# Performance work log

Measured on AMD Instinct MI355X. Metric: run time of the kernel, lower is better.

## Reference

```python
import jax, jax.numpy as jnp
import numpy as np


def setup_inputs() -> dict:
    key = jax.random.key(0)
    B, F, D = 16384, 26, 32
    inputs = jax.random.normal(key, (B, F, D), dtype=jnp.float32)
    return {"inputs": inputs}


def reference(inputs) -> jnp.ndarray:
    # inputs: [B, F, D]. Output: [B, F*(F-1)/2, D] of pairwise elementwise products,
    # ordered as (i, j) with i < j, i outer loop, j inner loop (matches tf double loop).
    F = inputs.shape[1]
    i_idx, j_idx = np.triu_indices(F, k=1)  # row-major order == original loop order
    # Single fused gather-multiply over index pairs.
    return inputs[:, i_idx, :] * inputs[:, j_idx, :]
```

## Files before the change

kernel.cpp:

```cpp
#include <hip/hip_runtime.h>

#define NF 26
#define ND 32
#define NPAIR 325
#define ROW_F4 (NF * ND / 4)
#define OUT_F4 (NPAIR * ND / 4)

__global__ __launch_bounds__(256) void interaction_kernel(
    const float4* __restrict__ in, float4* __restrict__ out)
{
    __shared__ float4 s_row[ROW_F4];
    __shared__ short  s_ai[NPAIR];
    __shared__ short  s_bj[NPAIR];

    const int b   = blockIdx.x;
    const int tid = threadIdx.x;

    if (tid < ROW_F4) s_row[tid] = in[b * ROW_F4 + tid];

    for (int p = tid; p < NPAIR; p += 256) {
        int i = 0, s = 0;
        while (s + (NF - 1 - i) <= p) { s += NF - 1 - i; ++i; }
        int j = p - s + i + 1;
        s_ai[p] = (short)(i * (ND / 4));
        s_bj[p] = (short)(j * (ND / 4));
    }
    __syncthreads();

    const int base = b * OUT_F4;
    for (int q = tid; q < OUT_F4; q += 256) {
        const int p  = q >> 3;
        const int d4 = q & 7;
        const float4 a = s_row[s_ai[p] + d4];
        const float4 v = s_row[s_bj[p] + d4];
        float4 r;
        r.x = a.x * v.x;
        r.y = a.y * v.y;
        r.z = a.z * v.z;
        r.w = a.w * v.w;
        out[base + q] = r;
    }
}

extern "C" void kernel_launch(void* const* d_in, const int* in_sizes, int n_in,
                              void* d_out, int out_size, void* d_ws, size_t ws_size,
                              hipStream_t stream) {
    const float4* in  = (const float4*)d_in[0];
    float4*       out = (float4*)d_out;
    const int B = in_sizes[0] / (NF * ND);
    interaction_kernel<<<B, 256, 0, stream>>>(in, out);
}
```

Baseline: 147.6 us.

## Process four rows per block with constant pair table and nontemporal stores

Replaces the per-block runtime computation of pair indices with a compile-time table in constant memory, and keeps each thread's source offsets in registers. Each block now handles four batch rows, which amortizes the table lookup and block setup. Output writes use nontemporal stores to reduce cache pollution on the large streaming output. The launch assumes the batch is divisible by four and gives fewer blocks, which lowers parallelism.

```diff
diff --git a/kernel.cpp b/kernel.cpp
--- a/kernel.cpp
+++ b/kernel.cpp
@@ -5,48 +5,74 @@
 #define NPAIR 325
 #define ROW_F4 (NF * ND / 4)
 #define OUT_F4 (NPAIR * ND / 4)
+#define ROWS 4
+#define NTHREADS 256
+#define KFULL (OUT_F4 / NTHREADS)
+#define KTAIL (OUT_F4 % NTHREADS)
 
-__global__ __launch_bounds__(256) void interaction_kernel(
-    const float4* __restrict__ in, float4* __restrict__ out)
+typedef float f32x4 __attribute__((ext_vector_type(4)));
+
+struct PairTab { unsigned short v[NPAIR]; };
+constexpr PairTab make_tab() {
+    PairTab t{};
+    int n = 0;
+    for (int i = 0; i < NF; ++i)
+        for (int j = i + 1; j < NF; ++j)
+            t.v[n++] = (unsigned short)((i * (ND / 4)) | ((j * (ND / 4)) << 8));
+    return t;
+}
+__constant__ PairTab c_tab = make_tab();
+
+__global__ __launch_bounds__(NTHREADS) void interaction_kernel(
+    const f32x4* __restrict__ in, f32x4* __restrict__ out)
 {
-    __shared__ float4 s_row[ROW_F4];
-    __shared__ short  s_ai[NPAIR];
-    __shared__ short  s_bj[NPAIR];
+    __shared__ f32x4 s_row[ROWS * ROW_F4];
 
-    const int b   = blockIdx.x;
+    const int b0  = blockIdx.x * ROWS;
     const int tid = threadIdx.x;
 
-    if (tid < ROW_F4) s_row[tid] = in[b * ROW_F4 + tid];
+    const f32x4* src = in + (size_t)b0 * ROW_F4;
+    for (int t = tid; t < ROWS * ROW_F4; t += NTHREADS)
+        s_row[t] = src[t];
 
-    for (int p = tid; p < NPAIR; p += 256) {
-        int i = 0, s = 0;
-        while (s + (NF - 1 - i) <= p) { s += NF - 1 - i; ++i; }
-        int j = p - s + i + 1;
-        s_ai[p] = (short)(i * (ND / 4));
-        s_bj[p] = (short)(j * (ND / 4));
+    int aoff[KFULL + 1], boff[KFULL + 1];
+    #pragma unroll
+    for (int k = 0; k <= KFULL; ++k) {
+        const int q = (k < KFULL) ? (tid + k * NTHREADS)
+                                  : (KFULL * NTHREADS + (tid < KTAIL ? tid : 0));
+        const unsigned int t = c_tab.v[q >> 3];
+        const int d = q & 7;
+        aoff[k] = (int)(t & 0xffu) + d;
+        boff[k] = (int)(t >> 8) + d;
     }
+
     __syncthreads();
 
-    const int base = b * OUT_F4;
-    for (int q = tid; q < OUT_F4; q += 256) {
-        const int p  = q >> 3;
-        const int d4 = q & 7;
-        const float4 a = s_row[s_ai[p] + d4];
-        const float4 v = s_row[s_bj[p] + d4];
-        float4 r;
-        r.x = a.x * v.x;
-        r.y = a.y * v.y;
-        r.z = a.z * v.z;
-        r.w = a.w * v.w;
-        out[base + q] = r;
+    #pragma unroll 1
+    for (int r = 0; r < ROWS; ++r) {
+        const f32x4* __restrict__ row = s_row + r * ROW_F4;
+        f32x4* __restrict__ dst = out + (size_t)(b0 + r) * OUT_F4;
+        #pragma unroll
+        for (int k = 0; k < KFULL; ++k) {
+            const f32x4 a = row[aoff[k]];
+            const f32x4 v = row[boff[k]];
+            const f32x4 rr = a * v;
+            __builtin_nontemporal_store(rr, dst + tid + k * NTHREADS);
+        }
+        if (tid < KTAIL) {
+            const f32x4 a = row[aoff[KFULL]];
+            const f32x4 v = row[boff[KFULL]];
+            const f32x4 rr = a * v;
+            __builtin_nontemporal_store(rr, dst + KFULL * NTHREADS + tid);
+        }
     }
 }
 
 extern "C" void kernel_launch(void* const* d_in, const int* in_sizes, int n_in,
                               void* d_out, int out_size, void* d_ws, size_t ws_size,
                               hipStream_t stream) {
-    const float4* in  = (const float4*)d_in[0];
-    float4*       out = (float4*)d_out;
+    const f32x4* in  = (const f32x4*)d_in[0];
+    f32x4*       out = (f32x4*)d_out;
     const int B = in_sizes[0] / (NF * ND);
-    interaction_kernel<<<B, 256, 0, stream>>>(in, out);
+    interaction_kernel<<<B / ROWS, NTHREADS, 0, stream>>>(in, out);
 }
```

New measurement: 141.6 us. 4.1% less time.

## Compute pair products from registers per row with nontemporal stores

Applied to the files above, without the earlier changes.

Replaces the shared-memory staging and index tables with a per-thread register copy of one row's 26 float4 slices. The pair loop is fully unrolled so each thread writes its product directly. Output is written with nontemporal stores to avoid polluting caches, and each wave handles 8 rows. This removes the LDS traffic, the syncthreads and the index computation, at the cost of higher register use and a grid that assumes B is divisible by 32.

```diff
diff --git a/kernel.cpp b/kernel.cpp
--- a/kernel.cpp
+++ b/kernel.cpp
@@ -5,48 +5,46 @@
 #define NPAIR 325
 #define ROW_F4 (NF * ND / 4)
 #define OUT_F4 (NPAIR * ND / 4)
+#define ROWS_PER_WAVE 8
+#define NTHREADS 256
+#define ROWS_PER_BLOCK (ROWS_PER_WAVE * NTHREADS / 64)
 
-__global__ __launch_bounds__(256) void interaction_kernel(
-    const float4* __restrict__ in, float4* __restrict__ out)
+typedef float f32x4 __attribute__((ext_vector_type(4)));
+
+__global__ __launch_bounds__(NTHREADS) void interaction_kernel(
+    const f32x4* __restrict__ in, f32x4* __restrict__ out)
 {
-    __shared__ float4 s_row[ROW_F4];
-    __shared__ short  s_ai[NPAIR];
-    __shared__ short  s_bj[NPAIR];
+    const int tid  = threadIdx.x;
+    const int wave = tid >> 6;
+    const int lane = tid & 63;
+    const int r    = lane >> 3;
+    const int d4   = lane & 7;
 
-    const int b   = blockIdx.x;
-    const int tid = threadIdx.x;
+    const long row = (long)blockIdx.x * ROWS_PER_BLOCK + wave * ROWS_PER_WAVE + r;
 
-    if (tid < ROW_F4) s_row[tid] = in[b * ROW_F4 + tid];
+    const f32x4* __restrict__ src = in + row * ROW_F4 + d4;
+    f32x4 a[NF];
+    #pragma unroll
+    for (int f = 0; f < NF; ++f) a[f] = src[f * (ND / 4)];
 
-    for (int p = tid; p < NPAIR; p += 256) {
-        int i = 0, s = 0;
-        while (s + (NF - 1 - i) <= p) { s += NF - 1 - i; ++i; }
-        int j = p - s + i + 1;
-        s_ai[p] = (short)(i * (ND / 4));
-        s_bj[p] = (short)(j * (ND / 4));
-    }
-    __syncthreads();
-
-    const int base = b * OUT_F4;
-    for (int q = tid; q < OUT_F4; q += 256) {
-        const int p  = q >> 3;
-        const int d4 = q & 7;
-        const float4 a = s_row[s_ai[p] + d4];
-        const float4 v = s_row[s_bj[p] + d4];
-        float4 r;
-        r.x = a.x * v.x;
-        r.y = a.y * v.y;
-        r.z = a.z * v.z;
-        r.w = a.w * v.w;
-        out[base + q] = r;
+    f32x4* __restrict__ dst = out + row * OUT_F4 + d4;
+    int p = 0;
+    #pragma unroll
+    for (int i = 0; i < NF; ++i) {
+        #pragma unroll
+        for (int j = i + 1; j < NF; ++j) {
+            __builtin_nontemporal_store(a[i] * a[j], dst + p * (ND / 4));
+            ++p;
+        }
     }
 }
 
 extern "C" void kernel_launch(void* const* d_in, const int* in_sizes, int n_in,
                               void* d_out, int out_size, void* d_ws, size_t ws_size,
                               hipStream_t stream) {
-    const float4* in  = (const float4*)d_in[0];
-    float4*       out = (float4*)d_out;
+    const f32x4* in  = (const f32x4*)d_in[0];
+    f32x4*       out = (f32x4*)d_out;
     const int B = in_sizes[0] / (NF * ND);
-    interaction_kernel<<<B, 256, 0, stream>>>(in, out);
+    const int blocks = B / ROWS_PER_BLOCK;
+    interaction_kernel<<<blocks, NTHREADS, 0, stream>>>(in, out);
 }
```

After: 138.8 us, median of 2. -6.0%, faster.
